# Kernel tuning notes

Hardware: AMD Instinct MI355X
Metric: run time of the kernel (lower is better)

## Reference

```python
import math
import jax, jax.numpy as jnp
import numpy as np

N_HEADS = 16
N_KV_HEADS = 4
HEAD_DIM = 128
D_MODEL = 2048
THETA = 10000.0
SCALE_BASE = 512


def _rope_cos_sin(seq_len, head_dim, theta):
    half = head_dim // 2
    inv_freq = 1.0 / theta ** (jnp.arange(half, dtype=jnp.float32) / half)
    pos = jnp.arange(seq_len, dtype=jnp.float32)
    freqs = jnp.outer(pos, inv_freq)  # (S, half)
    freqs = jnp.concatenate([freqs, freqs], axis=-1)  # (S, D)
    return jnp.cos(freqs), jnp.sin(freqs)


def _rotate_half(x):
    half = x.shape[-1] // 2
    return jnp.concatenate([-x[..., half:], x[..., :half]], axis=-1)


def _xpos_scale(seq_len, head_dim, scale_base):
    pos = jnp.arange(seq_len, dtype=jnp.float32)
    scale = (pos + scale_base / 2.0) / scale_base  # (S,)
    half = head_dim // 2
    s = jnp.broadcast_to(scale[:, None], (seq_len, half))
    # interleave: even idx -> scale, odd idx -> 1/scale
    return jnp.stack([s, 1.0 / s], axis=-1).reshape(seq_len, head_dim)


def setup_inputs() -> dict:
    key = jax.random.key(0)
    ks = jax.random.split(key, 5)
    std = 1.0 / math.sqrt(D_MODEL)
    x = jax.random.normal(ks[0], (2, 2048, D_MODEL), dtype=jnp.float32)
    Wq = jax.random.normal(ks[1], (D_MODEL, N_HEADS * HEAD_DIM), dtype=jnp.float32) * std
    Wk = jax.random.normal(ks[2], (D_MODEL, N_KV_HEADS * HEAD_DIM), dtype=jnp.float32) * std
    Wv = jax.random.normal(ks[3], (D_MODEL, N_KV_HEADS * HEAD_DIM), dtype=jnp.float32) * std
    Wo = jax.random.normal(ks[4], (N_HEADS * HEAD_DIM, D_MODEL), dtype=jnp.float32) * std
    return {"x": x, "Wq": Wq, "Wk": Wk, "Wv": Wv, "Wo": Wo}


def reference(x, Wq, Wk, Wv, Wo):
    B, S, _ = x.shape
    kv_groups = N_HEADS // N_KV_HEADS

    q = (x @ Wq).reshape(B, S, N_HEADS, HEAD_DIM).transpose(0, 2, 1, 3)     # (B,H,S,D)
    k = (x @ Wk).reshape(B, S, N_KV_HEADS, HEAD_DIM).transpose(0, 2, 1, 3)  # (B,Hk,S,D)
    v = (x @ Wv).reshape(B, S, N_KV_HEADS, HEAD_DIM).transpose(0, 2, 1, 3)

    cos, sin = _rope_cos_sin(S, HEAD_DIM, THETA)
    cos = cos[None, None]
    sin = sin[None, None]
    q = q * cos + _rotate_half(q) * sin
    k = k * cos + _rotate_half(k) * sin
    xscale = _xpos_scale(S, HEAD_DIM, SCALE_BASE)[None, None]
    q = q * xscale
    k = k * (1.0 / xscale)

    # GQA: expand kv heads to full head count
    k = jnp.repeat(k, kv_groups, axis=1)  # (B,H,S,D)
    v = jnp.repeat(v, kv_groups, axis=1)

    scale = math.sqrt(HEAD_DIM)
    scores = jnp.einsum('bhqd,bhkd->bhqk', q, k) / scale
    causal = jnp.tril(jnp.ones((S, S), dtype=bool))
    scores = jnp.where(causal[None, None], scores, -jnp.inf)
    attn = jax.nn.softmax(scores, axis=-1)
    out = jnp.einsum('bhqk,bhkd->bhqd', attn, v)
    out = out.transpose(0, 2, 1, 3).reshape(B, S, N_HEADS * HEAD_DIM)
    return out @ Wo
```

## Files before the change

### kernel.cpp

```cpp
#include <hip/hip_runtime.h>
#include <math.h>

#define BDIM 2
#define SLEN 2048
#define NH 16
#define NKV 4
#define HD 128

typedef __attribute__((ext_vector_type(8))) short short8v;
typedef __attribute__((ext_vector_type(4))) short short4v;
typedef __attribute__((ext_vector_type(8))) __bf16 bf16x8;
typedef __attribute__((ext_vector_type(4))) float f32x4;
typedef __attribute__((ext_vector_type(16))) float f32x16;
typedef __attribute__((ext_vector_type(4))) unsigned int u32x4;

__device__ inline unsigned short f2bf(float x) {
  unsigned int u = __builtin_bit_cast(unsigned int, x);
  unsigned int r = (u + 0x7fffu + ((u >> 16) & 1u)) >> 16;
  return (unsigned short)r;
}
__device__ inline float bf2f(unsigned short b) {
  unsigned int u = ((unsigned int)b) << 16;
  return __builtin_bit_cast(float, u);
}
__device__ inline unsigned int pk2(float a, float b) {
  unsigned short ua = __builtin_bit_cast(unsigned short, (__bf16)a);
  unsigned short ub = __builtin_bit_cast(unsigned short, (__bf16)b);
  return (unsigned int)ua | ((unsigned int)ub << 16);
}

template <bool BF16_OUT, bool SPLIT>
__global__ __launch_bounds__(256) void gemm_ring(
    const unsigned short* __restrict__ A, const unsigned short* __restrict__ Bt,
    void* __restrict__ C0, void* __restrict__ C1,
    int M, int N, int K, int Nsplit, int S0, int S1) {
  __shared__ __align__(16) unsigned short lds[3 * 8192];
  const int t    = threadIdx.x;
  const int lane = t & 63;
  const int w    = t >> 6;
  const int lg   = lane >> 4, l15 = lane & 15;
  const int wr   = w >> 1,    wc  = w & 1;
  const int bm = blockIdx.y * 128, bn = blockIdx.x * 128;

  const int r0  = t >> 2;
  const int c8  = (t & 3) ^ ((r0 >> 1) & 3);
  const int dst = t * 8;
  const int rk  = (l15 >> 1) & 3;

#define STAGE(kt, b)                                                           \
  { _Pragma("unroll") for (int i = 0; i < 2; ++i) {                            \
      __builtin_amdgcn_global_load_lds(                                        \
          (const __attribute__((address_space(1))) unsigned int*)              \
              &A[(size_t)(bm + i * 64 + r0) * K + (kt) * 32 + c8 * 8],         \
          (__attribute__((address_space(3))) unsigned int*)                    \
              &lds[(b) * 8192 + i * 2048 + dst],                               \
          16, 0, 0);                                                           \
      __builtin_amdgcn_global_load_lds(                                        \
          (const __attribute__((address_space(1))) unsigned int*)              \
              &Bt[(size_t)(bn + i * 64 + r0) * K + (kt) * 32 + c8 * 8],        \
          (__attribute__((address_space(3))) unsigned int*)                    \
              &lds[(b) * 8192 + 4096 + i * 2048 + dst],                        \
          16, 0, 0);                                                           \
  } }

  f32x4 acc[4][4];
#pragma unroll
  for (int m = 0; m < 4; ++m)
#pragma unroll
    for (int n = 0; n < 4; ++n) acc[m][n] = (f32x4){0.f, 0.f, 0.f, 0.f};

  const int NT = K >> 5;
  STAGE(0, 0)
  STAGE(1, 1)
  int bc = 0;

  for (int kt = 0; kt < NT; ++kt) {
    if (kt + 1 < NT) {
      asm volatile("s_waitcnt vmcnt(4)" ::: "memory");
    } else {
      asm volatile("s_waitcnt vmcnt(0)" ::: "memory");
    }
    __builtin_amdgcn_s_barrier();
    __builtin_amdgcn_sched_barrier(0);

    if (kt + 2 < NT) {
      const int nb = bc + 2 >= 3 ? bc - 1 : bc + 2;
      STAGE(kt + 2, nb)
    }

    const unsigned short* As = &lds[bc * 8192];
    const unsigned short* Bs = As + 4096;
    bf16x8 a[4], b[4];
#pragma unroll
    for (int m = 0; m < 4; ++m) {
      const int row = wr * 64 + m * 16 + l15;
      a[m] = __builtin_bit_cast(bf16x8, *reinterpret_cast<const short8v*>(
          &As[row * 32 + ((lg ^ rk) * 8)]));
    }
#pragma unroll
    for (int n = 0; n < 4; ++n) {
      const int row = wc * 64 + n * 16 + l15;
      b[n] = __builtin_bit_cast(bf16x8, *reinterpret_cast<const short8v*>(
          &Bs[row * 32 + ((lg ^ rk) * 8)]));
    }
#pragma unroll
    for (int m = 0; m < 4; ++m)
#pragma unroll
      for (int n = 0; n < 4; ++n)
        acc[m][n] = __builtin_amdgcn_mfma_f32_16x16x32_bf16(a[m], b[n], acc[m][n], 0, 0, 0);

    bc = (bc + 1 >= 3) ? 0 : bc + 1;
  }

  void* dst_p;
  int col0, stride;
  if (!SPLIT || bn < Nsplit) {
    dst_p = C0; col0 = bn; stride = S0;
  } else {
    dst_p = C1; col0 = bn - Nsplit; stride = S1;
  }
#pragma unroll
  for (int m = 0; m < 4; ++m) {
#pragma unroll
    for (int j = 0; j < 4; ++j) {
      const size_t row = (size_t)(bm + wr * 64 + m * 16 + lg * 4 + j);
#pragma unroll
      for (int n = 0; n < 4; ++n) {
        const int col = col0 + wc * 64 + n * 16 + l15;
        if (BF16_OUT)
          ((unsigned short*)dst_p)[row * stride + col] = f2bf(acc[m][n][j]);
        else
          ((float*)dst_p)[row * stride + col] = acc[m][n][j];
      }
    }
  }
#undef STAGE
}

__global__ __launch_bounds__(256) void prep_all(
    const float* __restrict__ x, const float* __restrict__ Wq,
    const float* __restrict__ Wk, const float* __restrict__ Wv,
    const float* __restrict__ Wo, unsigned short* __restrict__ xb,
    unsigned short* __restrict__ Wqkvt, unsigned short* __restrict__ Wot) {
  const int bx = blockIdx.x;
  if (bx >= 160) {
    const int cb = (bx - 160) * 64 + blockIdx.y;
    const int i = (cb * 256 + threadIdx.x) * 8;
    float4 a = *reinterpret_cast<const float4*>(&x[i]);
    float4 b = *reinterpret_cast<const float4*>(&x[i + 4]);
    short8v s;
    s[0] = f2bf(a.x); s[1] = f2bf(a.y); s[2] = f2bf(a.z); s[3] = f2bf(a.w);
    s[4] = f2bf(b.x); s[5] = f2bf(b.y); s[6] = f2bf(b.z); s[7] = f2bf(b.w);
    *reinterpret_cast<short8v*>(&xb[i]) = s;
    return;
  }
  const float* W;
  unsigned short* Wt;
  int N, nb;
  if (bx < 64)      { W = Wq; Wt = Wqkvt;                          N = 2048; nb = bx; }
  else if (bx < 80) { W = Wk; Wt = Wqkvt + (size_t)2048 * 2048;    N = 512;  nb = bx - 64; }
  else if (bx < 96) { W = Wv; Wt = Wqkvt + (size_t)2560 * 2048;    N = 512;  nb = bx - 80; }
  else              { W = Wo; Wt = Wot;                            N = 2048; nb = bx - 96; }
  const int K = 2048;
  __shared__ float tile[32][33];
  const int tx = threadIdx.x & 31, ty = threadIdx.x >> 5;
  const int n0 = nb * 32, k0 = blockIdx.y * 32;
#pragma unroll
  for (int i = 0; i < 4; ++i)
    tile[ty + i * 8][tx] = W[(size_t)(k0 + ty + i * 8) * N + n0 + tx];
  __syncthreads();
#pragma unroll
  for (int i = 0; i < 4; ++i)
    Wt[(size_t)(n0 + ty + i * 8) * K + k0 + tx] = f2bf(tile[tx][ty + i * 8]);
}

__global__ __launch_bounds__(256) void rope_tv_all(
    unsigned short* __restrict__ qb, unsigned short* __restrict__ kvb,
    unsigned short* __restrict__ vt) {
  const int bid = blockIdx.x;
  __shared__ unsigned short tile[64][136];
  if (bid >= 20480) {
    const int lb  = bid - 20480;
    const int st  = lb & 31;
    const int kvh = (lb >> 5) & 3;
    const int b   = lb >> 7;
    const int t = threadIdx.x;
#pragma unroll
    for (int i = 0; i < 4; ++i) {
      const int idx = t + i * 256;
      const int s   = idx >> 4;
      const int d0  = (idx & 15) * 8;
      short8v v = *reinterpret_cast<const short8v*>(
          &kvb[((size_t)(b * SLEN + st * 64 + s)) * 1024 + 512 + kvh * 128 + d0]);
      *reinterpret_cast<short8v*>(&tile[s][d0]) = v;
    }
    __syncthreads();
#pragma unroll
    for (int i = 0; i < 4; ++i) {
      const int idx = t + i * 256;
      const int d   = idx >> 3;
      const int cc  = idx & 7;
      const int cs  = cc ^ (d & 7);
      short8v o;
#pragma unroll
      for (int j = 0; j < 8; ++j) o[j] = (short)tile[cs * 8 + j][d];
      *reinterpret_cast<short8v*>(
          &vt[(((size_t)(b * 4 + kvh) * 128 + d) * 2048) + st * 64 + cc * 8]) = o;
    }
    return;
  }
  unsigned short* buf;
  int row_stride, nh_shift, invert, lbid;
  float extra_scale;
  if (bid < 16384) {
    buf = qb;  row_stride = 2048; nh_shift = 4; invert = 0;
    extra_scale = 0.088388347648318447f; lbid = bid;
  } else {
    buf = kvb; row_stride = 1024; nh_shift = 2; invert = 1;
    extra_scale = 1.0f; lbid = bid - 16384;
  }
  const int idx = lbid * 256 + threadIdx.x;
  const int dp  = idx & 63;
  const int tmp = idx >> 6;
  const int h   = tmp & ((1 << nh_shift) - 1);
  const int row = tmp >> nh_shift;
  const int s   = row & (SLEN - 1);

  const float inv_freq = expf(-(float)dp * (9.210340371976184f / 64.0f));
  const float ang = (float)s * inv_freq;
  float sn, cs;
  sincosf(ang, &sn, &cs);

  unsigned short* p = buf + (size_t)row * row_stride + h * HD;
  const float x0 = bf2f(p[dp]);
  const float x1 = bf2f(p[dp + 64]);
  float y0 = x0 * cs - x1 * sn;
  float y1 = x1 * cs + x0 * sn;

  const float scl = ((float)s + 256.0f) / 512.0f;
  float se_even = invert ? (1.0f / scl) : scl;
  float se_odd  = invert ? scl : (1.0f / scl);
  float se = ((dp & 1) ? se_odd : se_even) * extra_scale;

  p[dp]      = f2bf(y0 * se);
  p[dp + 64] = f2bf(y1 * se);
}

__global__ __launch_bounds__(512) void flash_attn_v12(
    const unsigned short* __restrict__ qb, const unsigned short* __restrict__ kvb,
    const unsigned short* __restrict__ vt, unsigned short* __restrict__ o) {
  const int bid = blockIdx.x;
  const int u   = bid & 7;
  const int bh  = bid >> 3;
  const int h   = bh & (NH - 1);
  const int b   = bh >> 4;
  const int kvh = h >> 2;

  __shared__ __align__(16) unsigned char smem[131072];

  const int t    = threadIdx.x;
  const int lane = t & 63;
  const int w    = t >> 6;
  const int par  = w >> 2;
  const int wq   = w & 3;
  const int hi   = lane >> 5;
  const int l31  = lane & 31;

  const size_t bS = (size_t)b * SLEN;
  const size_t vbase = (size_t)(b * 4 + kvh) * 128;

  int krow[2], kgrp[2];
#pragma unroll
  for (int i = 0; i < 2; ++i) {
    const int slot = w * 2048 + i * 1024 + lane * 16;
    krow[i] = slot >> 8;
    kgrp[i] = (slot >> 4) & 15;
  }
  int vrow[2], vchk[2];
#pragma unroll
  for (int i = 0; i < 2; ++i) {
    const int slot = w * 2048 + i * 1024 + lane * 16;
    vrow[i] = slot >> 7;
    vchk[i] = (slot >> 4) & 7;
  }

#define K_STAGE(kt, bufk)                                                      \
  { _Pragma("unroll") for (int i = 0; i < 2; ++i) {                            \
      const unsigned short* ksrc = &kvb[(bS + (size_t)(kt) * 64 + krow[i]) * 1024 \
          + kvh * 128 + ((kgrp[i] ^ (krow[i] & 15)) << 3)];                    \
      __builtin_amdgcn_global_load_lds(                                        \
          (const __attribute__((address_space(1))) unsigned int*)ksrc,         \
          (__attribute__((address_space(3))) unsigned int*)                    \
              (smem + (bufk) * 16384 + w * 2048 + i * 1024),                   \
          16, 0, 0); } }

#define V_STAGE(kt, bufk)                                                      \
  { _Pragma("unroll") for (int i = 0; i < 2; ++i) {                            \
      const unsigned short* vsrc = &vt[(vbase + vrow[i]) * 2048                \
          + (size_t)(kt) * 64 + vchk[i] * 8];                                  \
      __builtin_amdgcn_global_load_lds(                                        \
          (const __attribute__((address_space(1))) unsigned int*)vsrc,         \
          (__attribute__((address_space(3))) unsigned int*)                    \
              (smem + 65536 + (bufk) * 16384 + w * 2048 + i * 1024),           \
          16, 0, 0); } }

  for (int half = 0; half < 2; ++half) {
    const int qt2 = half ? (15 - u) : u;

    bf16x8 qf[8];
    {
      const size_t qrow = (bS + qt2 * 128 + wq * 32 + l31) * 2048 + (size_t)h * HD;
#pragma unroll
      for (int c = 0; c < 8; ++c)
        qf[c] = __builtin_bit_cast(bf16x8,
            *reinterpret_cast<const short8v*>(&qb[qrow + c * 16 + hi * 8]));
    }

    f32x16 Od[4];
#pragma unroll
    for (int ds = 0; ds < 4; ++ds)
#pragma unroll
      for (int r = 0; r < 16; ++r) Od[ds][r] = 0.f;
    float m_run = -1e30f, l_run = 0.f;

    K_STAGE(0, 0)
    K_STAGE(1, 1)
    V_STAGE(0, 0)
    V_STAGE(1, 1)
    __syncthreads();

    for (int e = 0; e <= qt2; ++e) {
      const int s = e & 1;
      const int kt = 2 * e + par;
      const bool more = (e < qt2);
      if (more) {
        K_STAGE(2 * e + 2, (s ^ 1) * 2 + 0)
        K_STAGE(2 * e + 3, (s ^ 1) * 2 + 1)
        V_STAGE(2 * e + 2, (s ^ 1) * 2 + 0)
        V_STAGE(2 * e + 3, (s ^ 1) * 2 + 1)
      }
      const unsigned short* Kb = (const unsigned short*)(smem + (s * 2 + par) * 16384);
      const unsigned int*   Vw = (const unsigned int*)(smem + 65536 + (s * 2 + par) * 16384);

      f32x16 Sa, Sb;
#pragma unroll
      for (int r = 0; r < 16; ++r) { Sa[r] = 0.f; Sb[r] = 0.f; }
      __builtin_amdgcn_s_setprio(1);
#pragma unroll
      for (int c = 0; c < 8; ++c) {
        const int ra = l31, rb = 32 + l31;
        bf16x8 ka = __builtin_bit_cast(bf16x8, *reinterpret_cast<const short8v*>(
            &Kb[ra * 128 + (((2 * c + hi) ^ (ra & 15)) << 3)]));
        bf16x8 kb2 = __builtin_bit_cast(bf16x8, *reinterpret_cast<const short8v*>(
            &Kb[rb * 128 + (((2 * c + hi) ^ (rb & 15)) << 3)]));
        Sa = __builtin_amdgcn_mfma_f32_32x32x16_bf16(ka, qf[c], Sa, 0, 0, 0);
        Sb = __builtin_amdgcn_mfma_f32_32x32x16_bf16(kb2, qf[c], Sb, 0, 0, 0);
      }
      __builtin_amdgcn_s_setprio(0);

      if (kt >= 2 * qt2) {
        const int thresh = qt2 * 128 + wq * 32 + l31 - kt * 64;
#pragma unroll
        for (int r = 0; r < 16; ++r) {
          const int kla = (r & 3) + 8 * (r >> 2) + 4 * hi;
          if (kla > thresh) Sa[r] = -INFINITY;
          if (kla + 32 > thresh) Sb[r] = -INFINITY;
        }
      }

      float pmax = Sa[0];
#pragma unroll
      for (int r = 0; r < 16; ++r) pmax = fmaxf(pmax, fmaxf(Sa[r], Sb[r]));
      pmax = fmaxf(pmax, __shfl_xor(pmax, 32));

      const bool defer = __all(pmax - m_run <= 8.0f);
      float m_new, f;
      if (defer) {
        m_new = m_run; f = 1.0f;
      } else {
        m_new = fmaxf(m_run, pmax);
        f = __expf(m_run - m_new);
        m_run = m_new;
      }

      float psum = 0.f;
#pragma unroll
      for (int r = 0; r < 16; ++r) {
        Sa[r] = __expf(Sa[r] - m_new);
        Sb[r] = __expf(Sb[r] - m_new);
        psum += Sa[r] + Sb[r];
      }
      psum += __shfl_xor(psum, 32);
      l_run = l_run * f + psum;

      if (!defer) {
#pragma unroll
        for (int ds = 0; ds < 4; ++ds)
#pragma unroll
          for (int r = 0; r < 16; ++r) Od[ds][r] *= f;
      }

#pragma unroll
      for (int kc = 0; kc < 4; ++kc) {
        const int Zz = kc & 1;
        f32x16 Sx = (kc >> 1) ? Sb : Sa;
        unsigned int W00 = pk2(Sx[4 * (2 * Zz + 0) + 0], Sx[4 * (2 * Zz + 0) + 1]);
        unsigned int W01 = pk2(Sx[4 * (2 * Zz + 0) + 2], Sx[4 * (2 * Zz + 0) + 3]);
        unsigned int W10 = pk2(Sx[4 * (2 * Zz + 1) + 0], Sx[4 * (2 * Zz + 1) + 1]);
        unsigned int W11 = pk2(Sx[4 * (2 * Zz + 1) + 2], Sx[4 * (2 * Zz + 1) + 3]);
        unsigned int X00 = __shfl_xor(W00, 32), X01 = __shfl_xor(W01, 32);
        unsigned int X10 = __shfl_xor(W10, 32), X11 = __shfl_xor(W11, 32);
        u32x4 pv;
        pv[0] = hi ? X10 : W00;
        pv[1] = hi ? X11 : W01;
        pv[2] = hi ? W10 : X00;
        pv[3] = hi ? W11 : X01;
        bf16x8 pf = __builtin_bit_cast(bf16x8, pv);
        __builtin_amdgcn_s_setprio(1);
#pragma unroll
        for (int ds = 0; ds < 4; ++ds) {
          const int d = ds * 32 + l31;
          u32x4 vv = *reinterpret_cast<const u32x4*>(
              &Vw[d * 32 + ((kc * 8 + hi * 4) ^ ((d & 7) << 2))]);
          bf16x8 vf = __builtin_bit_cast(bf16x8, vv);
          Od[ds] = __builtin_amdgcn_mfma_f32_32x32x16_bf16(vf, pf, Od[ds], 0, 0, 0);
        }
        __builtin_amdgcn_s_setprio(0);
      }

      __syncthreads();
    }

    float* mf = (float*)smem;
    float* Of = (float*)(smem + 2048);
    if (par == 1) {
      mf[(wq * 2 + 0) * 64 + lane] = m_run;
      mf[(wq * 2 + 1) * 64 + lane] = l_run;
    }
    float fe = 0.f, fo = 0.f, linv = 0.f;
#pragma unroll
    for (int p = 0; p < 2; ++p) {
      if (par == 1) {
#pragma unroll
        for (int d2 = 0; d2 < 2; ++d2)
#pragma unroll
          for (int r = 0; r < 16; ++r)
            Of[((wq * 2 + d2) * 16 + r) * 64 + lane] = Od[p * 2 + d2][r];
      }
      __syncthreads();
      if (par == 0) {
        if (p == 0) {
          const float m_o = mf[(wq * 2 + 0) * 64 + lane];
          const float l_o = mf[(wq * 2 + 1) * 64 + lane];
          const float mm = fmaxf(m_run, m_o);
          fe = __expf(m_run - mm);
          fo = __expf(m_o - mm);
          linv = 1.0f / (l_run * fe + l_o * fo);
        }
        const size_t row = bS + qt2 * 128 + wq * 32 + l31;
#pragma unroll
        for (int d2 = 0; d2 < 2; ++d2) {
          const int ds = p * 2 + d2;
#pragma unroll
          for (int g = 0; g < 4; ++g) {
            short4v ov;
#pragma unroll
            for (int j = 0; j < 4; ++j) {
              const int r = g * 4 + j;
              const float val = (Od[ds][r] * fe +
                                 Of[((wq * 2 + d2) * 16 + r) * 64 + lane] * fo) * linv;
              ov[j] = (short)__builtin_bit_cast(unsigned short, (__bf16)val);
            }
            const int dbase = ds * 32 + 8 * g + 4 * hi;
            *reinterpret_cast<short4v*>(&o[row * 2048 + h * HD + dbase]) = ov;
          }
        }
      }
      __syncthreads();
    }
  }
#undef K_STAGE
#undef V_STAGE
}

extern "C" void kernel_launch(void* const* d_in, const int* in_sizes, int n_in,
                              void* d_out, int out_size, void* d_ws, size_t ws_size,
                              hipStream_t stream) {
  (void)in_sizes; (void)n_in; (void)out_size; (void)ws_size;
  const float* x  = (const float*)d_in[0];
  const float* Wq = (const float*)d_in[1];
  const float* Wk = (const float*)d_in[2];
  const float* Wv = (const float*)d_in[3];
  const float* Wo = (const float*)d_in[4];
  float* out = (float*)d_out;

  unsigned char* ws = (unsigned char*)d_ws;
  const size_t MB = 1024 * 1024;
  unsigned short* xb    = (unsigned short*)(ws);
  unsigned short* Wqkvt = (unsigned short*)(ws + 16 * MB);
  unsigned short* Wot   = (unsigned short*)(ws + 28 * MB);
  unsigned short* qb    = (unsigned short*)(ws + 36 * MB);
  unsigned short* kvb   = (unsigned short*)(ws + 52 * MB);
  unsigned short* attn  = (unsigned short*)(ws + 60 * MB);
  unsigned short* vtb   = (unsigned short*)(ws + 76 * MB);

  const int M = BDIM * SLEN;
  dim3 blk(256);

  prep_all<<<dim3(224, 64), blk, 0, stream>>>(x, Wq, Wk, Wv, Wo, xb, Wqkvt, Wot);

  gemm_ring<true, true><<<dim3(24, 32), blk, 0, stream>>>(
      xb, Wqkvt, qb, kvb, M, 3072, 2048, 2048, 2048, 1024);

  rope_tv_all<<<20736, blk, 0, stream>>>(qb, kvb, vtb);

  flash_attn_v12<<<BDIM * NH * 8, dim3(512), 0, stream>>>(qb, kvb, vtb, attn);

  gemm_ring<false, false><<<dim3(16, 32), blk, 0, stream>>>(
      attn, Wot, out, nullptr, M, 2048, 2048, 2048, 2048, 0);
}
```

Measured before the change: 208.1 us.

## Fuse Q RoPE/xPos scaling into flash-attention Q load using precomputed cos/sin table

Q rotary embedding, xPos scaling and the softmax scale are now applied inside the attention kernel when Q fragments are loaded into registers. This removes the in-place Q rewrite pass over qb in the rope kernel, which now handles only K and the V transpose. A cos/sin table (2048x64 float2) is computed in the prep kernel and read from global memory. The cost is extra register pressure and global table reads in the attention prologue, plus Q values are rounded once from the GEMM's bf16 output rather than through the same path as before.

Result: no change. 210.1 us (+1.0%).

```diff
diff --git a/kernel.cpp b/kernel.cpp
--- a/kernel.cpp
+++ b/kernel.cpp
@@ -141,8 +141,19 @@
     const float* __restrict__ x, const float* __restrict__ Wq,
     const float* __restrict__ Wk, const float* __restrict__ Wv,
     const float* __restrict__ Wo, unsigned short* __restrict__ xb,
-    unsigned short* __restrict__ Wqkvt, unsigned short* __restrict__ Wot) {
+    unsigned short* __restrict__ Wqkvt, unsigned short* __restrict__ Wot,
+    float2* __restrict__ tab) {
   const int bx = blockIdx.x;
+  if (bx >= 224) {
+    const int idx = ((bx - 224) * 64 + blockIdx.y) * 256 + threadIdx.x;
+    const int spos = idx >> 6;
+    const int dp   = idx & 63;
+    const float inv_freq = expf(-(float)dp * (9.210340371976184f / 64.0f));
+    float sn, cs;
+    sincosf((float)spos * inv_freq, &sn, &cs);
+    tab[idx] = make_float2(cs, sn);
+    return;
+  }
   if (bx >= 160) {
     const int cb = (bx - 160) * 64 + blockIdx.y;
     const int i = (cb * 256 + threadIdx.x) * 8;
@@ -175,12 +186,11 @@
 }
 
 __global__ __launch_bounds__(256) void rope_tv_all(
-    unsigned short* __restrict__ qb, unsigned short* __restrict__ kvb,
-    unsigned short* __restrict__ vt) {
+    unsigned short* __restrict__ kvb, unsigned short* __restrict__ vt) {
   const int bid = blockIdx.x;
   __shared__ unsigned short tile[64][136];
-  if (bid >= 20480) {
-    const int lb  = bid - 20480;
+  if (bid >= 4096) {
+    const int lb  = bid - 4096;
     const int st  = lb & 31;
     const int kvh = (lb >> 5) & 3;
     const int b   = lb >> 7;
@@ -209,21 +219,11 @@
     }
     return;
   }
-  unsigned short* buf;
-  int row_stride, nh_shift, invert, lbid;
-  float extra_scale;
-  if (bid < 16384) {
-    buf = qb;  row_stride = 2048; nh_shift = 4; invert = 0;
-    extra_scale = 0.088388347648318447f; lbid = bid;
-  } else {
-    buf = kvb; row_stride = 1024; nh_shift = 2; invert = 1;
-    extra_scale = 1.0f; lbid = bid - 16384;
-  }
-  const int idx = lbid * 256 + threadIdx.x;
+  const int idx = bid * 256 + threadIdx.x;
   const int dp  = idx & 63;
   const int tmp = idx >> 6;
-  const int h   = tmp & ((1 << nh_shift) - 1);
-  const int row = tmp >> nh_shift;
+  const int h   = tmp & 3;
+  const int row = tmp >> 2;
   const int s   = row & (SLEN - 1);
 
   const float inv_freq = expf(-(float)dp * (9.210340371976184f / 64.0f));
@@ -231,24 +231,25 @@
   float sn, cs;
   sincosf(ang, &sn, &cs);
 
-  unsigned short* p = buf + (size_t)row * row_stride + h * HD;
+  unsigned short* p = kvb + (size_t)row * 1024 + h * HD;
   const float x0 = bf2f(p[dp]);
   const float x1 = bf2f(p[dp + 64]);
   float y0 = x0 * cs - x1 * sn;
   float y1 = x1 * cs + x0 * sn;
 
   const float scl = ((float)s + 256.0f) / 512.0f;
-  float se_even = invert ? (1.0f / scl) : scl;
-  float se_odd  = invert ? scl : (1.0f / scl);
-  float se = ((dp & 1) ? se_odd : se_even) * extra_scale;
+  const float se_even = 1.0f / scl;
+  const float se_odd  = scl;
+  const float se = (dp & 1) ? se_odd : se_even;
 
   p[dp]      = f2bf(y0 * se);
   p[dp + 64] = f2bf(y1 * se);
 }
 
-__global__ __launch_bounds__(512) void flash_attn_v12(
+__global__ __launch_bounds__(512) void flash_attn_v13(
     const unsigned short* __restrict__ qb, const unsigned short* __restrict__ kvb,
-    const unsigned short* __restrict__ vt, unsigned short* __restrict__ o) {
+    const unsigned short* __restrict__ vt, const float2* __restrict__ tab,
+    unsigned short* __restrict__ o) {
   const int bid = blockIdx.x;
   const int u   = bid & 7;
   const int bh  = bid >> 3;
@@ -309,11 +310,32 @@
 
     bf16x8 qf[8];
     {
-      const size_t qrow = (bS + qt2 * 128 + wq * 32 + l31) * 2048 + (size_t)h * HD;
+      const int spos = qt2 * 128 + wq * 32 + l31;
+      const size_t qrow = (bS + spos) * 2048 + (size_t)h * HD;
+      short8v qr[8];
 #pragma unroll
       for (int c = 0; c < 8; ++c)
-        qf[c] = __builtin_bit_cast(bf16x8,
-            *reinterpret_cast<const short8v*>(&qb[qrow + c * 16 + hi * 8]));
+        qr[c] = *reinterpret_cast<const short8v*>(&qb[qrow + c * 16 + hi * 8]);
+      const float scl = ((float)spos + 256.0f) / 512.0f;
+      const float se_e = scl * 0.088388347648318447f;
+      const float se_o = (1.0f / scl) * 0.088388347648318447f;
+      const float2* trow = &tab[spos * 64];
+#pragma unroll
+      for (int c = 0; c < 4; ++c) {
+        short8v nlo, nhi;
+#pragma unroll
+        for (int j = 0; j < 8; ++j) {
+          const int dp = c * 16 + hi * 8 + j;
+          const float2 cssn = trow[dp];
+          const float x0 = bf2f((unsigned short)qr[c][j]);
+          const float x1 = bf2f((unsigned short)qr[c + 4][j]);
+          const float se = (j & 1) ? se_o : se_e;
+          nlo[j] = (short)f2bf((x0 * cssn.x - x1 * cssn.y) * se);
+          nhi[j] = (short)f2bf((x1 * cssn.x + x0 * cssn.y) * se);
+        }
+        qf[c]     = __builtin_bit_cast(bf16x8, nlo);
+        qf[c + 4] = __builtin_bit_cast(bf16x8, nhi);
+      }
     }
 
     f32x16 Od[4];
@@ -503,18 +525,20 @@
   unsigned short* kvb   = (unsigned short*)(ws + 52 * MB);
   unsigned short* attn  = (unsigned short*)(ws + 60 * MB);
   unsigned short* vtb   = (unsigned short*)(ws + 76 * MB);
+  float2*         tab   = (float2*)(ws + 80 * MB);
 
   const int M = BDIM * SLEN;
   dim3 blk(256);
 
-  prep_all<<<dim3(224, 64), blk, 0, stream>>>(x, Wq, Wk, Wv, Wo, xb, Wqkvt, Wot);
+  prep_all<<<dim3(232, 64), blk, 0, stream>>>(
+      x, Wq, Wk, Wv, Wo, xb, Wqkvt, Wot, tab);
 
   gemm_ring<true, true><<<dim3(24, 32), blk, 0, stream>>>(
       xb, Wqkvt, qb, kvb, M, 3072, 2048, 2048, 2048, 1024);
 
-  rope_tv_all<<<20736, blk, 0, stream>>>(qb, kvb, vtb);
-
-  flash_attn_v12<<<BDIM * NH * 8, dim3(512), 0, stream>>>(qb, kvb, vtb, attn);
+  rope_tv_all<<<4352, blk, 0, stream>>>(kvb, vtb);
+
+  flash_attn_v13<<<BDIM * NH * 8, dim3(512), 0, stream>>>(qb, kvb, vtb, tab, attn);
 
   gemm_ring<false, false><<<dim3(16, 32), blk, 0, stream>>>(
       attn, Wot, out, nullptr, M, 2048, 2048, 2048, 2048, 0);
```
